# Kernel optimization log

Hardware: AMD Instinct MI355X
Metric: run time of the kernel (lower is better)

The kernel has to match this reference:

```python
import jax, jax.numpy as jnp
import numpy as np


def _layernorm(x, g, b, eps=1e-5):
    m = x.mean(-1, keepdims=True)
    v = ((x - m) ** 2).mean(-1, keepdims=True)
    return (x - m) * jax.lax.rsqrt(v + eps) * g + b


def _rmsnorm(x, w, eps=1e-6):
    return x * jax.lax.rsqrt((x * x).mean(-1, keepdims=True) + eps) * w


def setup_inputs() -> dict:
    key = jax.random.key(0)
    ks = jax.random.split(key, 8)
    B, T, S, C_img = 1, 3, 880, 3072
    C_mouse, D_hid, Dd = 2, 1024, 64
    vin = C_img + 12 * C_mouse  # 3096 = img_hidden + mouse_dim_in*vae_tcr*windows
    w = lambda k, shp: (jax.random.normal(k, shp, jnp.float32) * 0.02)
    return dict(
        x=jax.random.normal(ks[0], (B, T * S, C_img), jnp.float32),
        condition=jax.random.normal(ks[1], (B, 12, C_mouse), jnp.float32),
        w1=w(ks[2], (vin, D_hid)), b1=jnp.zeros((D_hid,), jnp.float32),
        w2=w(ks[3], (D_hid, D_hid)), b2=jnp.zeros((D_hid,), jnp.float32),
        ln_g=jnp.ones((D_hid,), jnp.float32), ln_b=jnp.zeros((D_hid,), jnp.float32),
        wqkv=w(ks[4], (D_hid, 3 * D_hid)), bqkv=jnp.zeros((3 * D_hid,), jnp.float32),
        qn_w=jnp.ones((Dd,), jnp.float32), kn_w=jnp.ones((Dd,), jnp.float32),
        wproj=w(ks[5], (D_hid, C_img)), bproj=jnp.zeros((C_img,), jnp.float32),
        H=22, W=40, temporal_shape=3, num_frame_per_block=3,
    )


def reference(x, condition, w1, b1, w2, b2, ln_g, ln_b, wqkv, bqkv,
              qn_w, kn_w, wproj, bproj, H, W, temporal_shape, num_frame_per_block):
    B, T_S, C_img = x.shape
    T = temporal_shape
    if condition.shape[1] > 9:
        condition = condition[:, -12:, :]
    _, N_frames, C = condition.shape
    action_len, pad_len = 20, 12
    pad = jnp.zeros((B, action_len - N_frames, C), condition.dtype)
    mouse_padded = jnp.concatenate([pad, condition], axis=1)  # [B, 20, C]
    # windowed gather: fixed small loop over num_frame_per_block (<=3)
    wins = jnp.stack([mouse_padded[:, i * 4:i * 4 + pad_len, :]
                      for i in range(num_frame_per_block)], axis=1)  # [B, F, 12, C]
    gm = wins.reshape(B, num_frame_per_block, pad_len * C)  # [B, F, 12C]
    S = 880  # hardcoded in original forward
    gm = jnp.broadcast_to(gm[:, None], (B, S, num_frame_per_block, pad_len * C))
    gm = gm.reshape(B * S, num_frame_per_block, pad_len * C)
    # fuse broadcast mouse features with image tokens (raw row-major reshape, as in torch)
    fused = jnp.concatenate([x.reshape(B * S, T, C_img), gm], axis=-1)  # [BS, T, C_img+12C]
    h = jax.nn.gelu(fused @ w1 + b1, approximate=True) @ w2 + b2
    h = _layernorm(h, ln_g, ln_b)  # [BS, T, D_hid]
    qkv = h @ wqkv + bqkv  # [BS, T, 3*D_hid]
    Dd = qn_w.shape[0]
    Hh = qkv.shape[-1] // (3 * Dd)
    qkv = qkv.reshape(B * S, T, 3, Hh, Dd)
    q, k, v = qkv[:, :, 0], qkv[:, :, 1], qkv[:, :, 2]
    q = _rmsnorm(q, qn_w).astype(v.dtype)
    k = _rmsnorm(k, kn_w).astype(v.dtype)
    # original flattens to one sequence of BS*T tokens for single_prefill (non-causal)
    N = B * S * T
    qf = q.reshape(N, Hh, Dd)
    kf = k.reshape(N, Hh, Dd)
    vf = v.reshape(N, Hh, Dd)
    scale = 1.0 / np.sqrt(Dd).astype(np.float32)
    scores = jnp.einsum('nhd,mhd->hnm', qf, kf) * scale  # [Hh, N, N]
    attn = jax.nn.softmax(scores, axis=-1)
    o = jnp.einsum('hnm,mhd->nhd', attn, vf)  # [N, Hh, Dd]
    # '(B S) T H D -> B (T S) (H D)'
    o = o.reshape(B, S, T, Hh, Dd).transpose(0, 2, 1, 3, 4).reshape(B, T * S, Hh * Dd)
    out = o @ wproj + bproj
    return x + out
```

## Files before the change

### kernel.cpp

```cpp
#include <hip/hip_runtime.h>
#include <hip/hip_bf16.h>

typedef __attribute__((ext_vector_type(8))) short short8;
typedef __attribute__((ext_vector_type(4))) short short4v;
typedef __attribute__((ext_vector_type(4))) float f32x4;
typedef __attribute__((ext_vector_type(16))) float f32x16;
typedef unsigned short u16;

#define ZERO16 (f32x16){0,0,0,0,0,0,0,0,0,0,0,0,0,0,0,0}

__device__ __forceinline__ float b2f(u16 h) {
    unsigned u = ((unsigned)h) << 16;
    float f; __builtin_memcpy(&f, &u, 4); return f;
}
__device__ __forceinline__ u16 f2b(float f) {
    __hip_bfloat16 h = __float2bfloat16(f);
    u16 r; __builtin_memcpy(&r, &h, 2); return r;
}
__device__ __forceinline__ void gload16(const void* g, void* l) {
    __builtin_amdgcn_global_load_lds(
        (const __attribute__((address_space(1))) unsigned*)g,
        (__attribute__((address_space(3))) unsigned*)l, 16, 0, 0);
}

#define M_VALID 2640
#define M_PAD   2688
#define K1      3096
#define K1P     3136
#define DH      1024
#define CIMG    3072
#define NHEAD   16
#define NT      84
#define QT      83
#define NSPLIT  3
#define TILES_PER_SPLIT 28

__global__ __launch_bounds__(256) void build_fused_kernel(
    const float* __restrict__ x, const float* __restrict__ cond,
    u16* __restrict__ fused)
{
    int n = blockIdx.x;
    int tid = threadIdx.x;
    const float* xr = x + (size_t)n * CIMG;
    u16* fr = fused + (size_t)n * K1P;
    for (int c = tid * 4; c < CIMG; c += 1024) {
        float4 v = *(const float4*)(xr + c);
        short4v w;
        w[0] = (short)f2b(v.x); w[1] = (short)f2b(v.y);
        w[2] = (short)f2b(v.z); w[3] = (short)f2b(v.w);
        *(short4v*)(fr + c) = w;
    }
    if (tid < 16) {
        int t = n % 3;
        short4v w;
        for (int jj = 0; jj < 4; jj++) {
            int j = tid * 4 + jj;
            float val = 0.f;
            if (j < 24) {
                int f = t * 4 + (j >> 1);
                if (f >= 8) val = cond[(f - 8) * 2 + (j & 1)];
            }
            w[jj] = (short)f2b(val);
        }
        *(short4v*)(fr + CIMG + tid * 4) = w;
    }
}

__global__ __launch_bounds__(256) void transpose_bf16_kernel(
    const float* __restrict__ W, u16* __restrict__ Wt, int K, int N, int ldt)
{
    __shared__ float t[32][33];
    int n0 = blockIdx.x * 32, k0 = blockIdx.y * 32;
    int x = threadIdx.x & 31, y0 = threadIdx.x >> 5;
    for (int yy = y0; yy < 32; yy += 8) {
        int k = k0 + yy, n = n0 + x;
        t[yy][x] = (k < K && n < N) ? W[(size_t)k * N + n] : 0.f;
    }
    __syncthreads();
    for (int yy = y0; yy < 32; yy += 8) {
        int n = n0 + yy, k = k0 + x;
        if (n < N && k < ldt) Wt[(size_t)n * ldt + k] = f2b(t[x][yy]);
    }
}

template<int EPI, int BM, int BN>
__global__ __launch_bounds__(256) void gemm_kernel(
    const u16* __restrict__ A, const u16* __restrict__ Bt,
    const float* __restrict__ bias, const float* __restrict__ resid,
    u16* __restrict__ Cb, float* __restrict__ Cf,
    int N, int K, int Mvalid)
{
    constexpr int MI  = BM / 32;
    constexpr int NJ  = BN / 32;
    constexpr int CA  = BM / 32;
    constexpr int CB  = BN / 32;
    constexpr unsigned ABYTES = BM * 128;
    constexpr unsigned BBYTES = BN * 128;
    constexpr unsigned STG = 2 * (ABYTES + BBYTES);
    constexpr unsigned CTW = BN + 4;
    constexpr unsigned CTB = BM * CTW * 4;
    __shared__ __align__(16) char smem[STG > CTB ? STG : CTB];

    const int tid = threadIdx.x;
    const int lane = tid & 63, wid = tid >> 6;
    const int l15 = lane & 15, l4 = lane >> 4;

    const int nx = N / BN;
    const int nwg = nx * (M_PAD / BM);
    const int bid = blockIdx.x;
    const int wgid = (bid & 7) * (nwg >> 3) + (bid >> 3);
    const int m0 = (wgid / nx) * BM, n0 = (wgid % nx) * BN;

    const int wr = (wid >> 1) * (BM / 2), wc = (wid & 1) * (BN / 2);

    const int srow = lane >> 3;
    const int scol = ((lane & 7) ^ (lane >> 3)) << 3;

    f32x4 acc[MI][NJ];
#pragma unroll
    for (int i = 0; i < MI; i++)
#pragma unroll
        for (int j = 0; j < NJ; j++) acc[i][j] = (f32x4){0.f, 0.f, 0.f, 0.f};

    const int nt = K >> 6;

    auto stage = [&](int buf, int k0) {
        char* Ab = smem + buf * ABYTES;
        char* Bb = smem + 2 * ABYTES + buf * BBYTES;
#pragma unroll
        for (int i = 0; i < CA; i++) {
            int c = wid * CA + i;
            gload16(A + (size_t)(m0 + c * 8 + srow) * K + k0 + scol,
                    Ab + c * 1024 + lane * 16);
        }
#pragma unroll
        for (int i = 0; i < CB; i++) {
            int c = wid * CB + i;
            gload16(Bt + (size_t)(n0 + c * 8 + srow) * K + k0 + scol,
                    Bb + c * 1024 + lane * 16);
        }
    };

    stage(0, 0);
    __syncthreads();
    int cur = 0;
    for (int t = 0; t < nt; t++) {
        if (t + 1 < nt) stage(cur ^ 1, (t + 1) * 64);
        const char* Ab = smem + cur * ABYTES;
        const char* Bb = smem + 2 * ABYTES + cur * BBYTES;
#pragma unroll
        for (int ki = 0; ki < 2; ki++) {
            short8 af[MI], bfr[NJ];
#pragma unroll
            for (int i = 0; i < MI; i++) {
                int row = wr + i * 16 + l15;
                af[i] = *(const short8*)(Ab + row * 128 + (((ki * 4 + l4) ^ (l15 & 7)) << 4));
            }
#pragma unroll
            for (int j = 0; j < NJ; j++) {
                int row = wc + j * 16 + l15;
                bfr[j] = *(const short8*)(Bb + row * 128 + (((ki * 4 + l4) ^ (l15 & 7)) << 4));
            }
#pragma unroll
            for (int i = 0; i < MI; i++)
#pragma unroll
                for (int j = 0; j < NJ; j++)
                    acc[i][j] = __builtin_amdgcn_mfma_f32_16x16x32_bf16(af[i], bfr[j], acc[i][j], 0, 0, 0);
        }
        __syncthreads();
        cur ^= 1;
    }

    float* Ct = (float*)smem;
#pragma unroll
    for (int i = 0; i < MI; i++)
#pragma unroll
        for (int j = 0; j < NJ; j++)
#pragma unroll
            for (int r = 0; r < 4; r++)
                Ct[(wr + i * 16 + l4 * 4 + r) * CTW + wc + j * 16 + l15] = acc[i][j][r];
    __syncthreads();

    const int row = tid >> 2;
    const int cb  = (tid & 3) * (BN / 4);
    const int grow = m0 + row;
    const int gcol = n0 + cb;
    if (EPI == 2) {
        if (grow < Mvalid) {
#pragma unroll
            for (int u = 0; u < BN / 16; u++) {
                f32x4 v = *(const f32x4*)&Ct[row * CTW + cb + u * 4];
                float4 bv = *(const float4*)&bias[gcol + u * 4];
                float4 rv = *(const float4*)&resid[(size_t)grow * N + gcol + u * 4];
                float4 o;
                o.x = v[0] + bv.x + rv.x; o.y = v[1] + bv.y + rv.y;
                o.z = v[2] + bv.z + rv.z; o.w = v[3] + bv.w + rv.w;
                *(float4*)&Cf[(size_t)grow * N + gcol + u * 4] = o;
            }
        }
    } else {
        u16 tmp[BN / 4];
#pragma unroll
        for (int u = 0; u < BN / 16; u++) {
            f32x4 v = *(const f32x4*)&Ct[row * CTW + cb + u * 4];
            float4 bv = *(const float4*)&bias[gcol + u * 4];
#pragma unroll
            for (int e = 0; e < 4; e++) {
                float val = v[e] + ((const float*)&bv)[e];
                if (EPI == 0) {
                    float tt = val + 0.044715f * val * val * val;
                    val = 0.5f * val * (1.0f + tanhf(0.7978845608028654f * tt));
                }
                tmp[u * 4 + e] = f2b(val);
            }
        }
#pragma unroll
        for (int u = 0; u < BN / 32; u++)
            *(short8*)(Cb + (size_t)grow * N + gcol + u * 8) = *(const short8*)&tmp[u * 8];
    }
}

__global__ __launch_bounds__(256) void ln_kernel(
    const u16* __restrict__ h2, const float* __restrict__ g,
    const float* __restrict__ b, u16* __restrict__ out)
{
    int row = blockIdx.x;
    int tid = threadIdx.x;
    const u16* p = h2 + (size_t)row * DH;
    float v[4];
#pragma unroll
    for (int i = 0; i < 4; i++) v[i] = b2f(p[tid * 4 + i]);
    float s1 = v[0] + v[1] + v[2] + v[3];
    float s2 = v[0]*v[0] + v[1]*v[1] + v[2]*v[2] + v[3]*v[3];
    for (int m = 1; m < 64; m <<= 1) { s1 += __shfl_xor(s1, m); s2 += __shfl_xor(s2, m); }
    __shared__ float a1[4], a2[4];
    int w = tid >> 6;
    if ((tid & 63) == 0) { a1[w] = s1; a2[w] = s2; }
    __syncthreads();
    s1 = a1[0] + a1[1] + a1[2] + a1[3];
    s2 = a2[0] + a2[1] + a2[2] + a2[3];
    float mean = s1 * (1.0f / 1024.0f);
    float var = s2 * (1.0f / 1024.0f) - mean * mean;
    float rs = rsqrtf(var + 1e-5f);
    u16* q = out + (size_t)row * DH;
#pragma unroll
    for (int i = 0; i < 4; i++) {
        int c = tid * 4 + i;
        q[c] = f2b((v[i] - mean) * rs * g[c] + b[c]);
    }
}

__global__ __launch_bounds__(256) void fragmentize_kernel(
    const u16* __restrict__ qkv, const float* __restrict__ qw, const float* __restrict__ kw,
    u16* __restrict__ Qf, u16* __restrict__ Kf, u16* __restrict__ Vf)
{
    __shared__ u16 Vlds[8 * 32 * 80];
    const int kt = blockIdx.x;
    const int hg = blockIdx.y;
    const int tid = threadIdx.x;
    const int t32 = tid >> 3, c8 = tid & 7;
    const int n = kt * 32 + t32;
    const u16* row = qkv + (size_t)n * 3072;

#pragma unroll
    for (int hh = 0; hh < 8; hh++) {
        short8 v = *(const short8*)(row + 2048 + (hg * 8 + hh) * 64 + c8 * 8);
        *(short8*)(&Vlds[(hh * 32 + t32) * 80 + c8 * 8]) = v;
    }

    float sq[8], sk[8];
#pragma unroll
    for (int hh = 0; hh < 8; hh++) {
        int h = hg * 8 + hh;
        short8 qv = *(const short8*)(row + h * 64 + c8 * 8);
        short8 kv = *(const short8*)(row + 1024 + h * 64 + c8 * 8);
        float aq = 0.f, ak = 0.f;
#pragma unroll
        for (int e = 0; e < 8; e++) {
            float fq = b2f((u16)qv[e]); aq += fq * fq;
            float fk = b2f((u16)kv[e]); ak += fk * fk;
        }
        sq[hh] = aq; sk[hh] = ak;
    }
#pragma unroll
    for (int m = 1; m < 8; m <<= 1) {
#pragma unroll
        for (int hh = 0; hh < 8; hh++) {
            sq[hh] += __shfl_xor(sq[hh], m);
            sk[hh] += __shfl_xor(sk[hh], m);
        }
    }

    float qwv[8], kwv[8];
#pragma unroll
    for (int e = 0; e < 8; e++) { qwv[e] = qw[c8 * 8 + e]; kwv[e] = kw[c8 * 8 + e]; }

#pragma unroll
    for (int hh = 0; hh < 8; hh++) {
        int h = hg * 8 + hh;
        float rq = rsqrtf(sq[hh] * (1.0f / 64.0f) + 1e-6f) * 0.125f;
        float rk = rsqrtf(sk[hh] * (1.0f / 64.0f) + 1e-6f);
        short8 qv = *(const short8*)(row + h * 64 + c8 * 8);
        short8 kv = *(const short8*)(row + 1024 + h * 64 + c8 * 8);
        short8 qo, ko;
#pragma unroll
        for (int e = 0; e < 8; e++) {
            qo[e] = (short)f2b(b2f((u16)qv[e]) * rq * qwv[e]);
            ko[e] = (short)f2b(b2f((u16)kv[e]) * rk * kwv[e]);
        }
        size_t base = (((size_t)(h * NT + kt) * 4 + (c8 >> 1)) << 9) + t32 * 16 + (c8 & 1) * 8;
        *(short8*)(Qf + base) = qo;
        *(short8*)(Kf + base) = ko;
    }

    __syncthreads();

    const int fd = tid >> 6;
    const int lkq = (tid & 63) >> 1, lhi = tid & 1;
#pragma unroll
    for (int hh = 0; hh < 8; hh++) {
        int h = hg * 8 + hh;
        short8 o;
#pragma unroll
        for (int e = 0; e < 8; e++)
            o[e] = (short)Vlds[(hh * 32 + (fd & 1) * 16 + lhi * 8 + e) * 80 + (fd >> 1) * 32 + lkq];
        *(short8*)(Vf + (((size_t)(h * NT + kt) * 4 + fd) << 9) + lkq * 16 + lhi * 8) = o;
    }
}

__device__ __forceinline__ void attn_tile(
    f32x16& st, float& mr, float& lr, f32x16& o0, f32x16& o1,
    u16* Pbuf, const short8* vv, int kq, int hi)
{
    float tmax = st[0];
#pragma unroll
    for (int r = 1; r < 16; r++) tmax = fmaxf(tmax, st[r]);
    tmax = fmaxf(tmax, __shfl_xor(tmax, 32));
    if (__any(tmax - mr > 8.0f)) {
        float mn = fmaxf(mr, tmax);
        float corr = __expf(mr - mn);
        mr = mn; lr *= corr;
#pragma unroll
        for (int r = 0; r < 16; r++) {
            float cr = __shfl(corr, (r & 3) + 8 * (r >> 2) + 4 * hi);
            o0[r] *= cr; o1[r] *= cr;
        }
    }
    float sum = 0.f;
    float p[16];
#pragma unroll
    for (int r = 0; r < 16; r++) { p[r] = __expf(st[r] - mr); sum += p[r]; }
    lr += sum + __shfl_xor(sum, 32);
#pragma unroll
    for (int g = 0; g < 4; g++) {
        short4v w;
#pragma unroll
        for (int e = 0; e < 4; e++) w[e] = (short)f2b(p[g * 4 + e]);
        *(short4v*)((char*)Pbuf + kq * 80 + g * 16 + hi * 8) = w;
    }
    short8 pa0 = *(const short8*)((const char*)Pbuf + kq * 80 + hi * 16);
    short8 pa1 = *(const short8*)((const char*)Pbuf + kq * 80 + 32 + hi * 16);
    o0 = __builtin_amdgcn_mfma_f32_32x32x16_bf16(pa0, vv[0], o0, 0, 0, 0);
    o0 = __builtin_amdgcn_mfma_f32_32x32x16_bf16(pa1, vv[1], o0, 0, 0, 0);
    o1 = __builtin_amdgcn_mfma_f32_32x32x16_bf16(pa0, vv[2], o1, 0, 0, 0);
    o1 = __builtin_amdgcn_mfma_f32_32x32x16_bf16(pa1, vv[3], o1, 0, 0, 0);
}

__global__ __launch_bounds__(64, 4) void attn_kernel(
    const u16* __restrict__ Qf, const u16* __restrict__ Kf,
    const u16* __restrict__ Vf, float* __restrict__ part, float* __restrict__ ml)
{
    __shared__ u16 P[32 * 40];
    const int bid = blockIdx.x;
    const int s   = bid / (NHEAD * QT);
    const int rem = bid % (NHEAD * QT);
    const int h   = rem / QT;
    const int qt  = rem % QT;
    const int lane = threadIdx.x;
    const int kq = lane & 31;
    const int hi = lane >> 5;
    const int q0 = qt * 32;
    const int lxy = kq * 16 + hi * 8;
    const u16* Kh = Kf + ((size_t)h * NT * 4 << 9);
    const u16* Vh = Vf + ((size_t)h * NT * 4 << 9);

    short8 qf[4];
#pragma unroll
    for (int d = 0; d < 4; d++)
        qf[d] = *(const short8*)(Qf + (((size_t)(h * NT + qt) * 4 + d) << 9) + lxy);

    f32x16 o0 = ZERO16, o1 = ZERO16;
    float mr = -3.0e38f, lr = 0.f;

    short8 kf[4];
#pragma unroll
    for (int d = 0; d < 4; d++)
        kf[d] = *(const short8*)(Kh + (((size_t)(s * TILES_PER_SPLIT) * 4 + d) << 9) + lxy);

    for (int i = 0; i < TILES_PER_SPLIT; i++) {
        const int tile = s * TILES_PER_SPLIT + i;
        const int k0 = tile * 32;
        short8 vv[4];
#pragma unroll
        for (int fd = 0; fd < 4; fd++)
            vv[fd] = *(const short8*)(Vh + (((size_t)tile * 4 + fd) << 9) + lxy);

        f32x16 st = ZERO16;
#pragma unroll
        for (int d = 0; d < 4; d++)
            st = __builtin_amdgcn_mfma_f32_32x32x16_bf16(kf[d], qf[d], st, 0, 0, 0);

        if (i < TILES_PER_SPLIT - 1) {
#pragma unroll
            for (int d = 0; d < 4; d++)
                kf[d] = *(const short8*)(Kh + (((size_t)(tile + 1) * 4 + d) << 9) + lxy);
        }

        if (k0 + 32 > M_VALID) {
#pragma unroll
            for (int r = 0; r < 16; r++) {
                int key = k0 + (r & 3) + 8 * (r >> 2) + 4 * hi;
                if (key >= M_VALID) st[r] = -3.0e38f;
            }
        }
        attn_tile(st, mr, lr, o0, o1, P, vv, kq, hi);
    }

#pragma unroll
    for (int r = 0; r < 16; r++) {
        int rl = (r & 3) + 8 * (r >> 2) + 4 * hi;
        int qrow = q0 + rl;
        if (qrow < M_VALID) {
            float* pp = part + ((size_t)s * M_PAD + qrow) * DH + h * 64;
            pp[kq] = o0[r];
            pp[kq + 32] = o1[r];
        }
    }
    if (hi == 0 && q0 + kq < M_VALID) {
        float* mlp = ml + (((size_t)s * NHEAD + h) * M_PAD + q0 + kq) * 2;
        mlp[0] = mr; mlp[1] = lr;
    }
}

__global__ __launch_bounds__(256) void attn_merge_kernel(
    const float* __restrict__ part, const float* __restrict__ ml, u16* __restrict__ obf)
{
    const int q = blockIdx.x;
    const int t = threadIdx.x;
    const int h = t >> 4, i = t & 15;
    float m[NSPLIT], l[NSPLIT];
#pragma unroll
    for (int s = 0; s < NSPLIT; s++) {
        const float* mlp = ml + (((size_t)s * NHEAD + h) * M_PAD + q) * 2;
        m[s] = mlp[0]; l[s] = mlp[1];
    }
    float M = fmaxf(fmaxf(m[0], m[1]), m[2]);
    float c[NSPLIT], L = 0.f;
#pragma unroll
    for (int s = 0; s < NSPLIT; s++) { c[s] = __expf(m[s] - M); L += c[s] * l[s]; }
    float inv = 1.0f / L;
    float4 acc = {0.f, 0.f, 0.f, 0.f};
#pragma unroll
    for (int s = 0; s < NSPLIT; s++) {
        float4 v = *(const float4*)(part + ((size_t)s * M_PAD + q) * DH + h * 64 + i * 4);
        acc.x += c[s] * v.x; acc.y += c[s] * v.y; acc.z += c[s] * v.z; acc.w += c[s] * v.w;
    }
    int mrow = (q % 3) * 880 + q / 3;
    short4v w;
    w[0] = (short)f2b(acc.x * inv); w[1] = (short)f2b(acc.y * inv);
    w[2] = (short)f2b(acc.z * inv); w[3] = (short)f2b(acc.w * inv);
    *(short4v*)(obf + (size_t)mrow * DH + h * 64 + i * 4) = w;
}

extern "C" void kernel_launch(void* const* d_in, const int* in_sizes, int n_in,
                              void* d_out, int out_size, void* d_ws, size_t ws_size,
                              hipStream_t stream)
{
    const float* x      = (const float*)d_in[0];
    const float* cond   = (const float*)d_in[1];
    const float* w1     = (const float*)d_in[2];
    const float* b1     = (const float*)d_in[3];
    const float* w2     = (const float*)d_in[4];
    const float* b2     = (const float*)d_in[5];
    const float* ln_g   = (const float*)d_in[6];
    const float* ln_b   = (const float*)d_in[7];
    const float* wqkv   = (const float*)d_in[8];
    const float* bqkv   = (const float*)d_in[9];
    const float* qn_w   = (const float*)d_in[10];
    const float* kn_w   = (const float*)d_in[11];
    const float* wproj  = (const float*)d_in[12];
    const float* bproj  = (const float*)d_in[13];
    float* out = (float*)d_out;

    char* ws = (char*)d_ws;
    size_t off = 0;
    auto alloc = [&](size_t bytes) { size_t o = off; off += (bytes + 255) & ~(size_t)255; return o; };

    size_t off_fused  = alloc((size_t)M_PAD * K1P * 2);
    size_t off_w1t    = alloc((size_t)DH * K1P * 2);
    size_t off_w2t    = alloc((size_t)DH * DH * 2);
    size_t off_wqkvt  = alloc((size_t)3072 * DH * 2);
    size_t off_wprojt = alloc((size_t)CIMG * DH * 2);
    size_t off_h1     = alloc((size_t)M_PAD * DH * 2);
    size_t off_h2     = alloc((size_t)M_PAD * DH * 2);
    size_t off_h2ln   = alloc((size_t)M_PAD * DH * 2);
    size_t off_qkv    = alloc((size_t)M_PAD * 3072 * 2);
    size_t off_qf     = alloc((size_t)NHEAD * NT * 4 * 512 * 2);
    size_t off_kf     = alloc((size_t)NHEAD * NT * 4 * 512 * 2);
    size_t off_vf     = alloc((size_t)NHEAD * NT * 4 * 512 * 2);
    size_t off_obf    = alloc((size_t)M_PAD * DH * 2);
    (void)ws_size;

    u16* fused  = (u16*)(ws + off_fused);
    u16* w1t    = (u16*)(ws + off_w1t);
    u16* w2t    = (u16*)(ws + off_w2t);
    u16* wqkvt  = (u16*)(ws + off_wqkvt);
    u16* wprojt = (u16*)(ws + off_wprojt);
    u16* h1     = (u16*)(ws + off_h1);
    u16* h2     = (u16*)(ws + off_h2);
    u16* h2ln   = (u16*)(ws + off_h2ln);
    u16* qkvb   = (u16*)(ws + off_qkv);
    u16* Qf     = (u16*)(ws + off_qf);
    u16* Kf     = (u16*)(ws + off_kf);
    u16* Vf     = (u16*)(ws + off_vf);
    u16* obf    = (u16*)(ws + off_obf);
    float* part = (float*)(ws + off_h1);
    float* mlbf = (float*)(ws + off_fused);

    hipMemsetAsync(ws + off_fused + (size_t)M_VALID * K1P * 2, 0, (size_t)(M_PAD - M_VALID) * K1P * 2, stream);

    build_fused_kernel<<<M_VALID, 256, 0, stream>>>(x, cond, fused);
    transpose_bf16_kernel<<<dim3(DH / 32, K1P / 32), 256, 0, stream>>>(w1, w1t, K1, DH, K1P);
    transpose_bf16_kernel<<<dim3(DH / 32, DH / 32), 256, 0, stream>>>(w2, w2t, DH, DH, DH);
    transpose_bf16_kernel<<<dim3(3072 / 32, DH / 32), 256, 0, stream>>>(wqkv, wqkvt, DH, 3072, DH);
    transpose_bf16_kernel<<<dim3(CIMG / 32, DH / 32), 256, 0, stream>>>(wproj, wprojt, DH, CIMG, DH);

    gemm_kernel<0, 64, 64><<<dim3((DH / 64) * (M_PAD / 64)), 256, 0, stream>>>(fused, w1t, b1, nullptr, h1, nullptr, DH, K1P, M_PAD);
    gemm_kernel<1, 64, 64><<<dim3((DH / 64) * (M_PAD / 64)), 256, 0, stream>>>(h1, w2t, b2, nullptr, h2, nullptr, DH, DH, M_PAD);
    ln_kernel<<<M_PAD, 256, 0, stream>>>(h2, ln_g, ln_b, h2ln);
    gemm_kernel<1, 64, 128><<<dim3((3072 / 128) * (M_PAD / 64)), 256, 0, stream>>>(h2ln, wqkvt, bqkv, nullptr, qkvb, nullptr, 3072, DH, M_PAD);
    fragmentize_kernel<<<dim3(NT, 2), 256, 0, stream>>>(qkvb, qn_w, kn_w, Qf, Kf, Vf);
    attn_kernel<<<dim3(NSPLIT * NHEAD * QT), 64, 0, stream>>>(Qf, Kf, Vf, part, mlbf);
    attn_merge_kernel<<<M_VALID, 256, 0, stream>>>(part, mlbf, obf);
    gemm_kernel<2, 64, 128><<<dim3((CIMG / 128) * (M_PAD / 64)), 256, 0, stream>>>(obf, wprojt, bproj, x, nullptr, out, CIMG, DH, M_VALID);
}
```

Measured before the change: 221.6 us.

## Register-permute P, use exp2, bf16 partials, two waves per attention block, setprio

Several attention-path changes land together. The softmax P tile no longer goes through an LDS round-trip; it is packed with v_cvt_pk_bf16_f32 and rearranged across half-waves with v_permlane32_swap. The log2e factor is folded into the Q scale so exp2 replaces expf, and split partial outputs are stored as bf16 instead of fp32, which halves merge traffic at some precision cost. The attention block now holds two waves covering two query tiles, and s_setprio is raised around MFMA bursts in both the attention kernel and the GEMM. QT=83 tiles become 42 pairs, so the last pair computes one padded tile beyond the 83 real ones.

```diff
diff --git a/kernel.cpp b/kernel.cpp
--- a/kernel.cpp
+++ b/kernel.cpp
@@ -3,6 +3,7 @@
 
 typedef __attribute__((ext_vector_type(8))) short short8;
 typedef __attribute__((ext_vector_type(4))) short short4v;
+typedef __attribute__((ext_vector_type(4))) unsigned uint4v;
 typedef __attribute__((ext_vector_type(4))) float f32x4;
 typedef __attribute__((ext_vector_type(16))) float f32x16;
 typedef unsigned short u16;
@@ -21,6 +22,11 @@
     __builtin_amdgcn_global_load_lds(
         (const __attribute__((address_space(1))) unsigned*)g,
         (__attribute__((address_space(3))) unsigned*)l, 16, 0, 0);
+}
+__device__ __forceinline__ unsigned cvtpk_bf16(float lo, float hi) {
+    unsigned d;
+    asm("v_cvt_pk_bf16_f32 %0, %1, %2" : "=v"(d) : "v"(lo), "v"(hi));
+    return d;
 }
 
 #define M_VALID 2640
@@ -31,9 +37,10 @@
 #define CIMG    3072
 #define NHEAD   16
 #define NT      84
-#define QT      83
+#define QTP     42
 #define NSPLIT  3
 #define TILES_PER_SPLIT 28
+#define LOG2E   1.4426950408889634f
 
 __global__ __launch_bounds__(256) void build_fused_kernel(
     const float* __restrict__ x, const float* __restrict__ cond,
@@ -161,11 +168,13 @@
                 int row = wc + j * 16 + l15;
                 bfr[j] = *(const short8*)(Bb + row * 128 + (((ki * 4 + l4) ^ (l15 & 7)) << 4));
             }
+            __builtin_amdgcn_s_setprio(1);
 #pragma unroll
             for (int i = 0; i < MI; i++)
 #pragma unroll
                 for (int j = 0; j < NJ; j++)
                     acc[i][j] = __builtin_amdgcn_mfma_f32_16x16x32_bf16(af[i], bfr[j], acc[i][j], 0, 0, 0);
+            __builtin_amdgcn_s_setprio(0);
         }
         __syncthreads();
         cur ^= 1;
@@ -298,7 +307,7 @@
 #pragma unroll
     for (int hh = 0; hh < 8; hh++) {
         int h = hg * 8 + hh;
-        float rq = rsqrtf(sq[hh] * (1.0f / 64.0f) + 1e-6f) * 0.125f;
+        float rq = rsqrtf(sq[hh] * (1.0f / 64.0f) + 1e-6f) * (0.125f * LOG2E);
         float rk = rsqrtf(sk[hh] * (1.0f / 64.0f) + 1e-6f);
         short8 qv = *(const short8*)(row + h * 64 + c8 * 8);
         short8 kv = *(const short8*)(row + 1024 + h * 64 + c8 * 8);
@@ -330,7 +339,7 @@
 
 __device__ __forceinline__ void attn_tile(
     f32x16& st, float& mr, float& lr, f32x16& o0, f32x16& o1,
-    u16* Pbuf, const short8* vv, int kq, int hi)
+    const short8* vv, int hi)
 {
     float tmax = st[0];
 #pragma unroll
@@ -338,7 +347,7 @@
     tmax = fmaxf(tmax, __shfl_xor(tmax, 32));
     if (__any(tmax - mr > 8.0f)) {
         float mn = fmaxf(mr, tmax);
-        float corr = __expf(mr - mn);
+        float corr = __builtin_amdgcn_exp2f(mr - mn);
         mr = mn; lr *= corr;
 #pragma unroll
         for (int r = 0; r < 16; r++) {
@@ -349,34 +358,42 @@
     float sum = 0.f;
     float p[16];
 #pragma unroll
-    for (int r = 0; r < 16; r++) { p[r] = __expf(st[r] - mr); sum += p[r]; }
+    for (int r = 0; r < 16; r++) { p[r] = __builtin_amdgcn_exp2f(st[r] - mr); sum += p[r]; }
     lr += sum + __shfl_xor(sum, 32);
-#pragma unroll
-    for (int g = 0; g < 4; g++) {
-        short4v w;
-#pragma unroll
-        for (int e = 0; e < 4; e++) w[e] = (short)f2b(p[g * 4 + e]);
-        *(short4v*)((char*)Pbuf + kq * 80 + g * 16 + hi * 8) = w;
-    }
-    short8 pa0 = *(const short8*)((const char*)Pbuf + kq * 80 + hi * 16);
-    short8 pa1 = *(const short8*)((const char*)Pbuf + kq * 80 + 32 + hi * 16);
+
+    unsigned a0 = cvtpk_bf16(p[0], p[1]),   a1 = cvtpk_bf16(p[2], p[3]);
+    unsigned a2 = cvtpk_bf16(p[4], p[5]),   a3 = cvtpk_bf16(p[6], p[7]);
+    unsigned a4 = cvtpk_bf16(p[8], p[9]),   a5 = cvtpk_bf16(p[10], p[11]);
+    unsigned a6 = cvtpk_bf16(p[12], p[13]), a7 = cvtpk_bf16(p[14], p[15]);
+    asm("v_permlane32_swap_b32 %0, %1" : "+v"(a0), "+v"(a2));
+    asm("v_permlane32_swap_b32 %0, %1" : "+v"(a1), "+v"(a3));
+    asm("v_permlane32_swap_b32 %0, %1" : "+v"(a4), "+v"(a6));
+    asm("v_permlane32_swap_b32 %0, %1" : "+v"(a5), "+v"(a7));
+    uint4v u0 = {a0, a1, a2, a3}, u1 = {a4, a5, a6, a7};
+    short8 pa0, pa1;
+    __builtin_memcpy(&pa0, &u0, 16);
+    __builtin_memcpy(&pa1, &u1, 16);
+
+    __builtin_amdgcn_s_setprio(1);
     o0 = __builtin_amdgcn_mfma_f32_32x32x16_bf16(pa0, vv[0], o0, 0, 0, 0);
     o0 = __builtin_amdgcn_mfma_f32_32x32x16_bf16(pa1, vv[1], o0, 0, 0, 0);
     o1 = __builtin_amdgcn_mfma_f32_32x32x16_bf16(pa0, vv[2], o1, 0, 0, 0);
     o1 = __builtin_amdgcn_mfma_f32_32x32x16_bf16(pa1, vv[3], o1, 0, 0, 0);
-}
-
-__global__ __launch_bounds__(64, 4) void attn_kernel(
+    __builtin_amdgcn_s_setprio(0);
+}
+
+__global__ __launch_bounds__(128, 4) void attn_kernel(
     const u16* __restrict__ Qf, const u16* __restrict__ Kf,
-    const u16* __restrict__ Vf, float* __restrict__ part, float* __restrict__ ml)
-{
-    __shared__ u16 P[32 * 40];
+    const u16* __restrict__ Vf, u16* __restrict__ part, float* __restrict__ ml)
+{
     const int bid = blockIdx.x;
-    const int s   = bid / (NHEAD * QT);
-    const int rem = bid % (NHEAD * QT);
-    const int h   = rem / QT;
-    const int qt  = rem % QT;
-    const int lane = threadIdx.x;
+    const int s   = bid / (NHEAD * QTP);
+    const int rem = bid % (NHEAD * QTP);
+    const int h   = rem / QTP;
+    const int qtp = rem % QTP;
+    const int wid = threadIdx.x >> 6;
+    const int qt  = qtp * 2 + wid;
+    const int lane = threadIdx.x & 63;
     const int kq = lane & 31;
     const int hi = lane >> 5;
     const int q0 = qt * 32;
@@ -406,9 +423,11 @@
             vv[fd] = *(const short8*)(Vh + (((size_t)tile * 4 + fd) << 9) + lxy);
 
         f32x16 st = ZERO16;
+        __builtin_amdgcn_s_setprio(1);
 #pragma unroll
         for (int d = 0; d < 4; d++)
             st = __builtin_amdgcn_mfma_f32_32x32x16_bf16(kf[d], qf[d], st, 0, 0, 0);
+        __builtin_amdgcn_s_setprio(0);
 
         if (i < TILES_PER_SPLIT - 1) {
 #pragma unroll
@@ -423,7 +442,7 @@
                 if (key >= M_VALID) st[r] = -3.0e38f;
             }
         }
-        attn_tile(st, mr, lr, o0, o1, P, vv, kq, hi);
+        attn_tile(st, mr, lr, o0, o1, vv, hi);
     }
 
 #pragma unroll
@@ -431,9 +450,9 @@
         int rl = (r & 3) + 8 * (r >> 2) + 4 * hi;
         int qrow = q0 + rl;
         if (qrow < M_VALID) {
-            float* pp = part + ((size_t)s * M_PAD + qrow) * DH + h * 64;
-            pp[kq] = o0[r];
-            pp[kq + 32] = o1[r];
+            u16* pp = part + ((size_t)s * M_PAD + qrow) * DH + h * 64;
+            pp[kq] = f2b(o0[r]);
+            pp[kq + 32] = f2b(o1[r]);
         }
     }
     if (hi == 0 && q0 + kq < M_VALID) {
@@ -443,7 +462,7 @@
 }
 
 __global__ __launch_bounds__(256) void attn_merge_kernel(
-    const float* __restrict__ part, const float* __restrict__ ml, u16* __restrict__ obf)
+    const u16* __restrict__ part, const float* __restrict__ ml, u16* __restrict__ obf)
 {
     const int q = blockIdx.x;
     const int t = threadIdx.x;
@@ -457,13 +476,14 @@
     float M = fmaxf(fmaxf(m[0], m[1]), m[2]);
     float c[NSPLIT], L = 0.f;
 #pragma unroll
-    for (int s = 0; s < NSPLIT; s++) { c[s] = __expf(m[s] - M); L += c[s] * l[s]; }
+    for (int s = 0; s < NSPLIT; s++) { c[s] = __builtin_amdgcn_exp2f(m[s] - M); L += c[s] * l[s]; }
     float inv = 1.0f / L;
     float4 acc = {0.f, 0.f, 0.f, 0.f};
 #pragma unroll
     for (int s = 0; s < NSPLIT; s++) {
-        float4 v = *(const float4*)(part + ((size_t)s * M_PAD + q) * DH + h * 64 + i * 4);
-        acc.x += c[s] * v.x; acc.y += c[s] * v.y; acc.z += c[s] * v.z; acc.w += c[s] * v.w;
+        short4v v = *(const short4v*)(part + ((size_t)s * M_PAD + q) * DH + h * 64 + i * 4);
+        acc.x += c[s] * b2f((u16)v[0]); acc.y += c[s] * b2f((u16)v[1]);
+        acc.z += c[s] * b2f((u16)v[2]); acc.w += c[s] * b2f((u16)v[3]);
     }
     int mrow = (q % 3) * 880 + q / 3;
     short4v w;
@@ -524,7 +544,7 @@
     u16* Kf     = (u16*)(ws + off_kf);
     u16* Vf     = (u16*)(ws + off_vf);
     u16* obf    = (u16*)(ws + off_obf);
-    float* part = (float*)(ws + off_h1);
+    u16* part   = (u16*)(ws + off_h1);
     float* mlbf = (float*)(ws + off_fused);
 
     hipMemsetAsync(ws + off_fused + (size_t)M_VALID * K1P * 2, 0, (size_t)(M_PAD - M_VALID) * K1P * 2, stream);
@@ -540,7 +560,7 @@
     ln_kernel<<<M_PAD, 256, 0, stream>>>(h2, ln_g, ln_b, h2ln);
     gemm_kernel<1, 64, 128><<<dim3((3072 / 128) * (M_PAD / 64)), 256, 0, stream>>>(h2ln, wqkvt, bqkv, nullptr, qkvb, nullptr, 3072, DH, M_PAD);
     fragmentize_kernel<<<dim3(NT, 2), 256, 0, stream>>>(qkvb, qn_w, kn_w, Qf, Kf, Vf);
-    attn_kernel<<<dim3(NSPLIT * NHEAD * QT), 64, 0, stream>>>(Qf, Kf, Vf, part, mlbf);
+    attn_kernel<<<dim3(NSPLIT * NHEAD * QTP), 128, 0, stream>>>(Qf, Kf, Vf, part, mlbf);
     attn_merge_kernel<<<M_VALID, 256, 0, stream>>>(part, mlbf, obf);
     gemm_kernel<2, 64, 128><<<dim3((CIMG / 128) * (M_PAD / 64)), 256, 0, stream>>>(obf, wprojt, bproj, x, nullptr, out, CIMG, DH, M_VALID);
 }
```

Measured after the change: 215.4 us. 2.8% less time.
